# Optimization experiments

Measured on AMD Instinct MI355X. Metric: run time of the kernel, lower is better.

## Reference

```python
import jax, jax.numpy as jnp
from jax import lax
import numpy as np

NUM_BINS = 16
EPS = 1e-8


def setup_inputs() -> dict:
    key = jax.random.key(0)
    x = jax.random.normal(key, (32, 512, 4096), dtype=jnp.float32)
    return {"x": x}


def reference(x):
    B, C, L = x.shape  # [B, C, L]
    nb = NUM_BINS
    # g = mean over sequence -> [B, C]
    g = x.mean(axis=2)
    # cosine similarity along channel dim between each column x[:, :, l] and g
    dot = jnp.einsum('bcl,bc->bl', x, g)                      # [B, L]
    xn = jnp.sqrt(jnp.sum(x * x, axis=1))                     # [B, L]
    gn = jnp.sqrt(jnp.sum(g * g, axis=1, keepdims=True))      # [B, 1]
    cos = dot / jnp.maximum(xn * gn, EPS)                     # [B, L]
    S = cos.reshape(-1)                                       # [B*L]
    # torch.linspace on tensor endpoints detaches -> stop_gradient for fidelity
    min_S = lax.stop_gradient(S.min())
    max_S = lax.stop_gradient(S.max())
    levels = min_S + jnp.arange(nb, dtype=S.dtype) * (max_S - min_S) / (nb - 1)  # [nb]
    # soft triangular binning: (1 - |S - L_n|) inside a half-width 0.5/nb window
    d = jnp.abs(S[:, None] - levels[None, :])                 # [B*L, nb]
    E = jnp.where(d < 0.5 / nb, 1.0 - d, 0.0)
    E = E.reshape(B, L, nb)
    count_map = E.sum(axis=1)                                 # [B, nb]
    count_map = count_map / count_map.sum(axis=1, keepdims=True)
    # adaptive_avg_pool1d from length 1 to C//nb just replicates the value
    out = jnp.broadcast_to(count_map[:, :, None], (B, nb, C // nb))
    return out
```

## Files before the change

### kernel.cpp

```cpp
#include <hip/hip_runtime.h>

typedef float f4 __attribute__((ext_vector_type(4)));

#define BB 32
#define CC 512
#define LL 4096
#define NB 16
#define EPSF 1e-8f

__global__ __launch_bounds__(256, 2)
void k_main(const float* __restrict__ x, float* __restrict__ g,
            f4* __restrict__ pd4, f4* __restrict__ ps4) {
    __shared__ f4 ldsD[1024], ldsS[1024];
    const int tid = threadIdx.x;
    const int w = tid >> 6, lane = tid & 63;
    const int b  = blockIdx.x >> 4;
    const int c0 = (blockIdx.x & 15) * 32;

    f4 dA[16], sA[16];
#pragma unroll
    for (int i = 0; i < 16; ++i) { dA[i] = (f4)0.f; sA[i] = (f4)0.f; }

    const f4* base = (const f4*)(x + ((size_t)b * CC + c0 + w * 8) * LL);
    for (int cc = 0; cc < 8; ++cc) {
        const f4* row = base + (size_t)cc * 1024;
        f4 v[16];
#pragma unroll
        for (int i = 0; i < 16; ++i) v[i] = row[i * 64 + lane];
        float s = 0.f;
#pragma unroll
        for (int i = 0; i < 16; ++i) s += (v[i][0] + v[i][1]) + (v[i][2] + v[i][3]);
#pragma unroll
        for (int off = 32; off; off >>= 1) s += __shfl_down(s, off, 64);
        s = __shfl(s, 0, 64);
        const float gv = s * (1.0f / LL);
        if (lane == 0) g[b * CC + c0 + w * 8 + cc] = gv;
#pragma unroll
        for (int i = 0; i < 16; ++i) {
#pragma unroll
            for (int k = 0; k < 4; ++k) {
                dA[i][k] = fmaf(v[i][k], gv, dA[i][k]);
                sA[i][k] = fmaf(v[i][k], v[i][k], sA[i][k]);
            }
        }
    }
    for (int ww = 0; ww < 4; ++ww) {
        if (w == ww) {
#pragma unroll
            for (int i = 0; i < 16; ++i) {
                const int idx = i * 64 + lane;
                if (ww == 0) { ldsD[idx] = dA[i];  ldsS[idx] = sA[i]; }
                else         { ldsD[idx] += dA[i]; ldsS[idx] += sA[i]; }
            }
        }
        __syncthreads();
    }
#pragma unroll
    for (int j = 0; j < 4; ++j) {
        pd4[(size_t)blockIdx.x * 1024 + j * 256 + tid] = ldsD[j * 256 + tid];
        ps4[(size_t)blockIdx.x * 1024 + j * 256 + tid] = ldsS[j * 256 + tid];
    }
}

__global__ __launch_bounds__(256, 8)
void k_reduce(const float* __restrict__ g,
              const f4* __restrict__ pd4, const f4* __restrict__ ps4,
              f4* __restrict__ cosv4,
              float* __restrict__ pmin, float* __restrict__ pmax) {
    const int tid = threadIdx.x;
    const int w = tid >> 6, lane = tid & 63;
    const int b = blockIdx.x >> 4;
    const int sl = (blockIdx.x & 15) * 64 + lane;

    f4 pdv = (f4)0.f, psv = (f4)0.f;
    const size_t cb = (size_t)b * 16;
#pragma unroll
    for (int c = 0; c < 4; ++c) {
        const int ch = 4 * w + c;
        pdv += pd4[((cb + ch) << 10) + sl];
        psv += ps4[((cb + ch) << 10) + sl];
    }
    __shared__ f4 sD[4][64], sS[4][64];
    sD[w][lane] = pdv;
    sS[w][lane] = psv;

    const f4* g4p = (const f4*)(g + b * CC);
    f4 ga = g4p[lane], gb2 = g4p[64 + lane];
    float sq = 0.f;
#pragma unroll
    for (int k = 0; k < 4; ++k) sq = fmaf(ga[k], ga[k], fmaf(gb2[k], gb2[k], sq));
#pragma unroll
    for (int off = 32; off; off >>= 1) sq += __shfl_down(sq, off, 64);
    const float gn = sqrtf(__shfl(sq, 0, 64));

    __syncthreads();
    if (tid < 64) {
        f4 d = ((sD[0][lane] + sD[1][lane]) + sD[2][lane]) + sD[3][lane];
        f4 ssum = ((sS[0][lane] + sS[1][lane]) + sS[2][lane]) + sS[3][lane];
        f4 cs;
#pragma unroll
        for (int k = 0; k < 4; ++k)
            cs[k] = d[k] / fmaxf(sqrtf(ssum[k]) * gn, EPSF);
        cosv4[(size_t)b * 1024 + sl] = cs;

        float mn = fminf(fminf(cs[0], cs[1]), fminf(cs[2], cs[3]));
        float mx = fmaxf(fmaxf(cs[0], cs[1]), fmaxf(cs[2], cs[3]));
#pragma unroll
        for (int off = 32; off; off >>= 1) {
            mn = fminf(mn, __shfl_down(mn, off, 64));
            mx = fmaxf(mx, __shfl_down(mx, off, 64));
        }
        if (lane == 0) { pmin[blockIdx.x] = mn; pmax[blockIdx.x] = mx; }
    }
}

__global__ void k_hist(const float* __restrict__ cosv,
                       const float* __restrict__ pmin, const float* __restrict__ pmax,
                       float* __restrict__ out) {
    const int b = blockIdx.x;
    const int wave = threadIdx.x >> 6, lane = threadIdx.x & 63;

    float mn = fminf(pmin[threadIdx.x], pmin[threadIdx.x + 256]);
    float mx = fmaxf(pmax[threadIdx.x], pmax[threadIdx.x + 256]);
#pragma unroll
    for (int off = 32; off; off >>= 1) {
        mn = fminf(mn, __shfl_down(mn, off, 64));
        mx = fmaxf(mx, __shfl_down(mx, off, 64));
    }
    __shared__ float smn[4], smx[4];
    if (lane == 0) { smn[wave] = mn; smx[wave] = mx; }
    __syncthreads();
    mn = fminf(fminf(smn[0], smn[1]), fminf(smn[2], smn[3]));
    mx = fmaxf(fmaxf(smx[0], smx[1]), fmaxf(smx[2], smx[3]));
    const float range = mx - mn;

    float bins[NB];
#pragma unroll
    for (int n = 0; n < NB; ++n) bins[n] = 0.f;

    const float* cb = cosv + (b << 12);
    for (int l = threadIdx.x; l < LL; l += 256) {
        float s = cb[l];
#pragma unroll
        for (int n = 0; n < NB; ++n) {
            float lev = mn + ((float)n * range) / 15.0f;
            float d = fabsf(s - lev);
            bins[n] += (d < 0.03125f) ? (1.0f - d) : 0.f;
        }
    }
#pragma unroll
    for (int n = 0; n < NB; ++n) {
#pragma unroll
        for (int off = 32; off; off >>= 1) bins[n] += __shfl_down(bins[n], off, 64);
    }
    __shared__ float sb[4][NB];
    if (lane == 0) {
#pragma unroll
        for (int n = 0; n < NB; ++n) sb[wave][n] = bins[n];
    }
    __syncthreads();
    __shared__ float colsum[NB];
    if (threadIdx.x < NB) {
        const int n = threadIdx.x;
        colsum[n] = sb[0][n] + sb[1][n] + sb[2][n] + sb[3][n];
    }
    __syncthreads();
    float total = 0.f;
#pragma unroll
    for (int n = 0; n < NB; ++n) total += colsum[n];
    {
        const int i0 = threadIdx.x;
        out[b * (NB * 32) + i0]       = colsum[i0 >> 5] / total;
        out[b * (NB * 32) + i0 + 256] = colsum[(i0 + 256) >> 5] / total;
    }
}

extern "C" void kernel_launch(void* const* d_in, const int* in_sizes, int n_in,
                              void* d_out, int out_size, void* d_ws, size_t ws_size,
                              hipStream_t stream) {
    const float* x = (const float*)d_in[0];
    float* out = (float*)d_out;
    float* ws  = (float*)d_ws;

    float* g    = ws;
    float* cosv = ws + 16384;
    float* pmin = ws + 16384 + 131072;
    float* pmax = pmin + 512;
    f4*    pd4  = (f4*)(pmax + 512);
    f4*    ps4  = pd4 + 524288;

    k_main<<<512, 256, 0, stream>>>(x, g, pd4, ps4);
    k_reduce<<<512, 256, 0, stream>>>(g, pd4, ps4, (f4*)cosv, pmin, pmax);
    k_hist<<<32, 256, 0, stream>>>(cosv, pmin, pmax, out);
}
```

Baseline: 66.09 us.

## Prefetch next channel row via register double-buffering with LDS staging

```diff
diff --git a/kernel.cpp b/kernel.cpp
--- a/kernel.cpp
+++ b/kernel.cpp
@@ -11,7 +11,7 @@
 __global__ __launch_bounds__(256, 2)
 void k_main(const float* __restrict__ x, float* __restrict__ g,
             f4* __restrict__ pd4, f4* __restrict__ ps4) {
-    __shared__ f4 ldsD[1024], ldsS[1024];
+    __shared__ f4 buf[4][1024];
     const int tid = threadIdx.x;
     const int w = tid >> 6, lane = tid & 63;
     const int b  = blockIdx.x >> 4;
@@ -22,14 +22,28 @@
     for (int i = 0; i < 16; ++i) { dA[i] = (f4)0.f; sA[i] = (f4)0.f; }
 
     const f4* base = (const f4*)(x + ((size_t)b * CC + c0 + w * 8) * LL);
+    f4* wb = buf[w];
+
+    f4 v[16];
+#pragma unroll
+    for (int i = 0; i < 16; ++i) v[i] = base[i * 64 + lane];
+
     for (int cc = 0; cc < 8; ++cc) {
-        const f4* row = base + (size_t)cc * 1024;
-        f4 v[16];
-#pragma unroll
-        for (int i = 0; i < 16; ++i) v[i] = row[i * 64 + lane];
         float s = 0.f;
 #pragma unroll
-        for (int i = 0; i < 16; ++i) s += (v[i][0] + v[i][1]) + (v[i][2] + v[i][3]);
+        for (int i = 0; i < 16; ++i) {
+            wb[i * 64 + lane] = v[i];
+#pragma unroll
+            for (int k = 0; k < 4; ++k)
+                sA[i][k] = fmaf(v[i][k], v[i][k], sA[i][k]);
+            s += (v[i][0] + v[i][1]) + (v[i][2] + v[i][3]);
+        }
+        if (cc < 7) {
+            const f4* nr = base + (size_t)(cc + 1) * 1024;
+#pragma unroll
+            for (int i = 0; i < 16; ++i) v[i] = nr[i * 64 + lane];
+        }
+        __builtin_amdgcn_sched_barrier(0);
 #pragma unroll
         for (int off = 32; off; off >>= 1) s += __shfl_down(s, off, 64);
         s = __shfl(s, 0, 64);
@@ -37,13 +51,15 @@
         if (lane == 0) g[b * CC + c0 + w * 8 + cc] = gv;
 #pragma unroll
         for (int i = 0; i < 16; ++i) {
-#pragma unroll
-            for (int k = 0; k < 4; ++k) {
-                dA[i][k] = fmaf(v[i][k], gv, dA[i][k]);
-                sA[i][k] = fmaf(v[i][k], v[i][k], sA[i][k]);
-            }
-        }
-    }
+            f4 f = wb[i * 64 + lane];
+#pragma unroll
+            for (int k = 0; k < 4; ++k)
+                dA[i][k] = fmaf(f[k], gv, dA[i][k]);
+        }
+    }
+    __syncthreads();
+    f4* ldsD = &buf[0][0];
+    f4* ldsS = &buf[2][0];
     for (int ww = 0; ww < 4; ++ww) {
         if (w == ww) {
 #pragma unroll
@@ -114,7 +130,7 @@
     }
 }
 
-__global__ void k_hist(const float* __restrict__ cosv,
+__global__ void k_hist(const f4* __restrict__ cosv4,
                        const float* __restrict__ pmin, const float* __restrict__ pmax,
                        float* __restrict__ out) {
     const int b = blockIdx.x;
@@ -138,14 +154,19 @@
 #pragma unroll
     for (int n = 0; n < NB; ++n) bins[n] = 0.f;
 
-    const float* cb = cosv + (b << 12);
-    for (int l = threadIdx.x; l < LL; l += 256) {
-        float s = cb[l];
-#pragma unroll
-        for (int n = 0; n < NB; ++n) {
-            float lev = mn + ((float)n * range) / 15.0f;
-            float d = fabsf(s - lev);
-            bins[n] += (d < 0.03125f) ? (1.0f - d) : 0.f;
+    const f4* cb = cosv4 + b * 1024;
+#pragma unroll
+    for (int j = 0; j < 4; ++j) {
+        f4 sv = cb[j * 256 + threadIdx.x];
+#pragma unroll
+        for (int k = 0; k < 4; ++k) {
+            const float s = sv[k];
+#pragma unroll
+            for (int n = 0; n < NB; ++n) {
+                float lev = mn + ((float)n * range) / 15.0f;
+                float d = fabsf(s - lev);
+                bins[n] += (d < 0.03125f) ? (1.0f - d) : 0.f;
+            }
         }
     }
 #pragma unroll
@@ -191,5 +212,5 @@
 
     k_main<<<512, 256, 0, stream>>>(x, g, pd4, ps4);
     k_reduce<<<512, 256, 0, stream>>>(g, pd4, ps4, (f4*)cosv, pmin, pmax);
-    k_hist<<<32, 256, 0, stream>>>(cosv, pmin, pmax, out);
-}
+    k_hist<<<32, 256, 0, stream>>>((const f4*)cosv, pmin, pmax, out);
+}
```

After: 98.15 us. 48.5% more time.

## Fuse reduce and histogram kernels using a grid-wide atomic barrier

Applied to the files above, without the earlier changes.

```diff
diff --git a/kernel.cpp b/kernel.cpp
--- a/kernel.cpp
+++ b/kernel.cpp
@@ -62,27 +62,22 @@
     }
 }
 
-__global__ __launch_bounds__(256, 8)
-void k_reduce(const float* __restrict__ g,
-              const f4* __restrict__ pd4, const f4* __restrict__ ps4,
-              f4* __restrict__ cosv4,
-              float* __restrict__ pmin, float* __restrict__ pmax) {
+__global__ __launch_bounds__(1024, 1)
+void k_rh(const float* __restrict__ g,
+          const f4* __restrict__ pd4, const f4* __restrict__ ps4,
+          float* __restrict__ pmin, float* __restrict__ pmax,
+          unsigned* __restrict__ counter, float* __restrict__ out) {
+    const int b = blockIdx.x;
     const int tid = threadIdx.x;
     const int w = tid >> 6, lane = tid & 63;
-    const int b = blockIdx.x >> 4;
-    const int sl = (blockIdx.x & 15) * 64 + lane;
 
     f4 pdv = (f4)0.f, psv = (f4)0.f;
     const size_t cb = (size_t)b * 16;
 #pragma unroll
-    for (int c = 0; c < 4; ++c) {
-        const int ch = 4 * w + c;
-        pdv += pd4[((cb + ch) << 10) + sl];
-        psv += ps4[((cb + ch) << 10) + sl];
+    for (int ch = 0; ch < 16; ++ch) {
+        pdv += pd4[((cb + ch) << 10) + tid];
+        psv += ps4[((cb + ch) << 10) + tid];
     }
-    __shared__ f4 sD[4][64], sS[4][64];
-    sD[w][lane] = pdv;
-    sS[w][lane] = psv;
 
     const f4* g4p = (const f4*)(g + b * CC);
     f4 ga = g4p[lane], gb2 = g4p[64 + lane];
@@ -93,57 +88,55 @@
     for (int off = 32; off; off >>= 1) sq += __shfl_down(sq, off, 64);
     const float gn = sqrtf(__shfl(sq, 0, 64));
 
-    __syncthreads();
-    if (tid < 64) {
-        f4 d = ((sD[0][lane] + sD[1][lane]) + sD[2][lane]) + sD[3][lane];
-        f4 ssum = ((sS[0][lane] + sS[1][lane]) + sS[2][lane]) + sS[3][lane];
-        f4 cs;
+    f4 cs;
 #pragma unroll
-        for (int k = 0; k < 4; ++k)
-            cs[k] = d[k] / fmaxf(sqrtf(ssum[k]) * gn, EPSF);
-        cosv4[(size_t)b * 1024 + sl] = cs;
+    for (int k = 0; k < 4; ++k)
+        cs[k] = pdv[k] / fmaxf(sqrtf(psv[k]) * gn, EPSF);
 
-        float mn = fminf(fminf(cs[0], cs[1]), fminf(cs[2], cs[3]));
-        float mx = fmaxf(fmaxf(cs[0], cs[1]), fmaxf(cs[2], cs[3]));
-#pragma unroll
-        for (int off = 32; off; off >>= 1) {
-            mn = fminf(mn, __shfl_down(mn, off, 64));
-            mx = fmaxf(mx, __shfl_down(mx, off, 64));
-        }
-        if (lane == 0) { pmin[blockIdx.x] = mn; pmax[blockIdx.x] = mx; }
-    }
-}
-
-__global__ void k_hist(const float* __restrict__ cosv,
-                       const float* __restrict__ pmin, const float* __restrict__ pmax,
-                       float* __restrict__ out) {
-    const int b = blockIdx.x;
-    const int wave = threadIdx.x >> 6, lane = threadIdx.x & 63;
-
-    float mn = fminf(pmin[threadIdx.x], pmin[threadIdx.x + 256]);
-    float mx = fmaxf(pmax[threadIdx.x], pmax[threadIdx.x + 256]);
+    float mn = fminf(fminf(cs[0], cs[1]), fminf(cs[2], cs[3]));
+    float mx = fmaxf(fmaxf(cs[0], cs[1]), fmaxf(cs[2], cs[3]));
 #pragma unroll
     for (int off = 32; off; off >>= 1) {
         mn = fminf(mn, __shfl_down(mn, off, 64));
         mx = fmaxf(mx, __shfl_down(mx, off, 64));
     }
-    __shared__ float smn[4], smx[4];
-    if (lane == 0) { smn[wave] = mn; smx[wave] = mx; }
+    __shared__ float smn[16], smx[16];
+    if (lane == 0) { smn[w] = mn; smx[w] = mx; }
     __syncthreads();
-    mn = fminf(fminf(smn[0], smn[1]), fminf(smn[2], smn[3]));
-    mx = fmaxf(fmaxf(smx[0], smx[1]), fmaxf(smx[2], smx[3]));
-    const float range = mx - mn;
+    if (tid == 0) {
+        float bmn = smn[0], bmx = smx[0];
+#pragma unroll
+        for (int i = 1; i < 16; ++i) { bmn = fminf(bmn, smn[i]); bmx = fmaxf(bmx, smx[i]); }
+        pmin[b] = bmn; pmax[b] = bmx;
+        __threadfence();
+        atomicAdd(counter, 1u);
+    }
+    if (tid == 0) {
+        while (__hip_atomic_load(counter, __ATOMIC_ACQUIRE, __HIP_MEMORY_SCOPE_AGENT) < 32u)
+            __builtin_amdgcn_s_sleep(2);
+    }
+    __syncthreads();
+
+    __shared__ float lmn[32], lmx[32];
+    if (tid < 32) {
+        lmn[tid] = __hip_atomic_load(&pmin[tid], __ATOMIC_RELAXED, __HIP_MEMORY_SCOPE_AGENT);
+        lmx[tid] = __hip_atomic_load(&pmax[tid], __ATOMIC_RELAXED, __HIP_MEMORY_SCOPE_AGENT);
+    }
+    __syncthreads();
+    float gmn = lmn[0], gmx = lmx[0];
+#pragma unroll
+    for (int i = 1; i < 32; ++i) { gmn = fminf(gmn, lmn[i]); gmx = fmaxf(gmx, lmx[i]); }
+    const float range = gmx - gmn;
 
     float bins[NB];
 #pragma unroll
     for (int n = 0; n < NB; ++n) bins[n] = 0.f;
-
-    const float* cb = cosv + (b << 12);
-    for (int l = threadIdx.x; l < LL; l += 256) {
-        float s = cb[l];
+#pragma unroll
+    for (int k = 0; k < 4; ++k) {
+        const float s = cs[k];
 #pragma unroll
         for (int n = 0; n < NB; ++n) {
-            float lev = mn + ((float)n * range) / 15.0f;
+            float lev = gmn + ((float)n * range) / 15.0f;
             float d = fabsf(s - lev);
             bins[n] += (d < 0.03125f) ? (1.0f - d) : 0.f;
         }
@@ -153,25 +146,25 @@
 #pragma unroll
         for (int off = 32; off; off >>= 1) bins[n] += __shfl_down(bins[n], off, 64);
     }
-    __shared__ float sb[4][NB];
+    __shared__ float sb[16][NB];
     if (lane == 0) {
 #pragma unroll
-        for (int n = 0; n < NB; ++n) sb[wave][n] = bins[n];
+        for (int n = 0; n < NB; ++n) sb[w][n] = bins[n];
     }
     __syncthreads();
     __shared__ float colsum[NB];
-    if (threadIdx.x < NB) {
-        const int n = threadIdx.x;
-        colsum[n] = sb[0][n] + sb[1][n] + sb[2][n] + sb[3][n];
+    if (tid < NB) {
+        float c = 0.f;
+#pragma unroll
+        for (int i = 0; i < 16; ++i) c += sb[i][tid];
+        colsum[tid] = c;
     }
     __syncthreads();
-    float total = 0.f;
+    if (tid < NB * 32) {
+        float total = 0.f;
 #pragma unroll
-    for (int n = 0; n < NB; ++n) total += colsum[n];
-    {
-        const int i0 = threadIdx.x;
-        out[b * (NB * 32) + i0]       = colsum[i0 >> 5] / total;
-        out[b * (NB * 32) + i0 + 256] = colsum[(i0 + 256) >> 5] / total;
+        for (int n = 0; n < NB; ++n) total += colsum[n];
+        out[b * (NB * 32) + tid] = colsum[tid >> 5] / total;
     }
 }
 
@@ -182,14 +175,14 @@
     float* out = (float*)d_out;
     float* ws  = (float*)d_ws;
 
-    float* g    = ws;
-    float* cosv = ws + 16384;
-    float* pmin = ws + 16384 + 131072;
-    float* pmax = pmin + 512;
-    f4*    pd4  = (f4*)(pmax + 512);
-    f4*    ps4  = pd4 + 524288;
+    float*    g       = ws;
+    float*    pmin    = ws + 16384;
+    float*    pmax    = ws + 16384 + 64;
+    unsigned* counter = (unsigned*)(ws + 16384 + 128);
+    f4*       pd4     = (f4*)(ws + 16384 + 256);
+    f4*       ps4     = pd4 + 524288;
 
+    hipMemsetAsync(counter, 0, sizeof(unsigned), stream);
     k_main<<<512, 256, 0, stream>>>(x, g, pd4, ps4);
-    k_reduce<<<512, 256, 0, stream>>>(g, pd4, ps4, (f4*)cosv, pmin, pmax);
-    k_hist<<<32, 256, 0, stream>>>(cosv, pmin, pmax, out);
+    k_rh<<<32, 1024, 0, stream>>>(g, pd4, ps4, pmin, pmax, counter, out);
 }
```

Measured after the change: 74.17 us. 1.12x slower.

## Fuse reduce and histogram kernels using grid-wide atomic barriers

Applied to the files above, without the earlier changes.

```diff
diff --git a/kernel.cpp b/kernel.cpp
--- a/kernel.cpp
+++ b/kernel.cpp
@@ -62,11 +62,12 @@
     }
 }
 
-__global__ __launch_bounds__(256, 8)
-void k_reduce(const float* __restrict__ g,
-              const f4* __restrict__ pd4, const f4* __restrict__ ps4,
-              f4* __restrict__ cosv4,
-              float* __restrict__ pmin, float* __restrict__ pmax) {
+__global__ __launch_bounds__(256)
+void k_rh(const float* __restrict__ g,
+          const f4* __restrict__ pd4, const f4* __restrict__ ps4,
+          float* __restrict__ pmin, float* __restrict__ pmax,
+          float* __restrict__ bblk, unsigned* __restrict__ counters,
+          float* __restrict__ out) {
     const int tid = threadIdx.x;
     const int w = tid >> 6, lane = tid & 63;
     const int b = blockIdx.x >> 4;
@@ -94,82 +95,94 @@
     const float gn = sqrtf(__shfl(sq, 0, 64));
 
     __syncthreads();
+    f4 cs = (f4)0.f;
+    float mn = 1e30f, mx = -1e30f;
     if (tid < 64) {
         f4 d = ((sD[0][lane] + sD[1][lane]) + sD[2][lane]) + sD[3][lane];
         f4 ssum = ((sS[0][lane] + sS[1][lane]) + sS[2][lane]) + sS[3][lane];
-        f4 cs;
 #pragma unroll
         for (int k = 0; k < 4; ++k)
             cs[k] = d[k] / fmaxf(sqrtf(ssum[k]) * gn, EPSF);
-        cosv4[(size_t)b * 1024 + sl] = cs;
-
-        float mn = fminf(fminf(cs[0], cs[1]), fminf(cs[2], cs[3]));
-        float mx = fmaxf(fmaxf(cs[0], cs[1]), fmaxf(cs[2], cs[3]));
+        mn = fminf(fminf(cs[0], cs[1]), fminf(cs[2], cs[3]));
+        mx = fmaxf(fmaxf(cs[0], cs[1]), fmaxf(cs[2], cs[3]));
 #pragma unroll
         for (int off = 32; off; off >>= 1) {
             mn = fminf(mn, __shfl_down(mn, off, 64));
             mx = fmaxf(mx, __shfl_down(mx, off, 64));
         }
-        if (lane == 0) { pmin[blockIdx.x] = mn; pmax[blockIdx.x] = mx; }
-    }
-}
-
-__global__ void k_hist(const float* __restrict__ cosv,
-                       const float* __restrict__ pmin, const float* __restrict__ pmax,
-                       float* __restrict__ out) {
-    const int b = blockIdx.x;
-    const int wave = threadIdx.x >> 6, lane = threadIdx.x & 63;
-
-    float mn = fminf(pmin[threadIdx.x], pmin[threadIdx.x + 256]);
-    float mx = fmaxf(pmax[threadIdx.x], pmax[threadIdx.x + 256]);
+    }
+    if (tid == 0) {
+        pmin[blockIdx.x] = mn;
+        pmax[blockIdx.x] = mx;
+        __threadfence();
+        atomicAdd(&counters[0], 1u);
+        while (__hip_atomic_load(&counters[0], __ATOMIC_ACQUIRE, __HIP_MEMORY_SCOPE_AGENT) < 512u)
+            __builtin_amdgcn_s_sleep(2);
+    }
+    __syncthreads();
+
+    float m0 = fminf(pmin[tid], pmin[tid + 256]);
+    float m1 = fmaxf(pmax[tid], pmax[tid + 256]);
 #pragma unroll
     for (int off = 32; off; off >>= 1) {
-        mn = fminf(mn, __shfl_down(mn, off, 64));
-        mx = fmaxf(mx, __shfl_down(mx, off, 64));
+        m0 = fminf(m0, __shfl_down(m0, off, 64));
+        m1 = fmaxf(m1, __shfl_down(m1, off, 64));
     }
     __shared__ float smn[4], smx[4];
-    if (lane == 0) { smn[wave] = mn; smx[wave] = mx; }
-    __syncthreads();
-    mn = fminf(fminf(smn[0], smn[1]), fminf(smn[2], smn[3]));
-    mx = fmaxf(fmaxf(smx[0], smx[1]), fmaxf(smx[2], smx[3]));
-    const float range = mx - mn;
-
-    float bins[NB];
-#pragma unroll
-    for (int n = 0; n < NB; ++n) bins[n] = 0.f;
-
-    const float* cb = cosv + (b << 12);
-    for (int l = threadIdx.x; l < LL; l += 256) {
-        float s = cb[l];
+    if (lane == 0) { smn[w] = m0; smx[w] = m1; }
+    __syncthreads();
+    const float gmn = fminf(fminf(smn[0], smn[1]), fminf(smn[2], smn[3]));
+    const float gmx = fmaxf(fmaxf(smx[0], smx[1]), fmaxf(smx[2], smx[3]));
+    const float range = gmx - gmn;
+
+    if (tid < 64) {
+        float bins[NB];
+#pragma unroll
+        for (int n = 0; n < NB; ++n) bins[n] = 0.f;
+#pragma unroll
+        for (int k = 0; k < 4; ++k) {
+            const float s = cs[k];
+#pragma unroll
+            for (int n = 0; n < NB; ++n) {
+                float lev = gmn + ((float)n * range) / 15.0f;
+                float d = fabsf(s - lev);
+                bins[n] += (d < 0.03125f) ? (1.0f - d) : 0.f;
+            }
+        }
 #pragma unroll
         for (int n = 0; n < NB; ++n) {
-            float lev = mn + ((float)n * range) / 15.0f;
-            float d = fabsf(s - lev);
-            bins[n] += (d < 0.03125f) ? (1.0f - d) : 0.f;
-        }
-    }
-#pragma unroll
-    for (int n = 0; n < NB; ++n) {
-#pragma unroll
-        for (int off = 32; off; off >>= 1) bins[n] += __shfl_down(bins[n], off, 64);
-    }
-    __shared__ float sb[4][NB];
-    if (lane == 0) {
-#pragma unroll
-        for (int n = 0; n < NB; ++n) sb[wave][n] = bins[n];
-    }
-    __syncthreads();
+#pragma unroll
+            for (int off = 32; off; off >>= 1) bins[n] += __shfl_down(bins[n], off, 64);
+        }
+        if (lane == 0) {
+#pragma unroll
+            for (int n = 0; n < NB; ++n) bblk[blockIdx.x * NB + n] = bins[n];
+            __threadfence();
+            atomicAdd(&counters[1], 1u);
+        }
+    }
+    if ((blockIdx.x & 15) != 0) return;
+
+    if (tid == 0) {
+        while (__hip_atomic_load(&counters[1], __ATOMIC_ACQUIRE, __HIP_MEMORY_SCOPE_AGENT) < 512u)
+            __builtin_amdgcn_s_sleep(2);
+    }
+    __syncthreads();
+
     __shared__ float colsum[NB];
-    if (threadIdx.x < NB) {
-        const int n = threadIdx.x;
-        colsum[n] = sb[0][n] + sb[1][n] + sb[2][n] + sb[3][n];
+    if (tid < NB) {
+        float c = 0.f;
+#pragma unroll
+        for (int ch = 0; ch < 16; ++ch)
+            c += bblk[(b * 16 + ch) * NB + tid];
+        colsum[tid] = c;
     }
     __syncthreads();
     float total = 0.f;
 #pragma unroll
     for (int n = 0; n < NB; ++n) total += colsum[n];
     {
-        const int i0 = threadIdx.x;
+        const int i0 = tid;
         out[b * (NB * 32) + i0]       = colsum[i0 >> 5] / total;
         out[b * (NB * 32) + i0 + 256] = colsum[(i0 + 256) >> 5] / total;
     }
@@ -182,14 +195,16 @@
     float* out = (float*)d_out;
     float* ws  = (float*)d_ws;
 
-    float* g    = ws;
-    float* cosv = ws + 16384;
-    float* pmin = ws + 16384 + 131072;
-    float* pmax = pmin + 512;
-    f4*    pd4  = (f4*)(pmax + 512);
-    f4*    ps4  = pd4 + 524288;
-
+    float*    g        = ws;
+    float*    pmin     = ws + 16384;
+    float*    pmax     = pmin + 512;
+    unsigned* counters = (unsigned*)(pmax + 512);
+    float*    bblk     = (float*)(counters + 16);
+    f4*       pd4      = (f4*)(bblk + 8192);
+    f4*       ps4      = pd4 + 524288;
+
+    hipMemsetAsync(counters, 0, 64, stream);
     k_main<<<512, 256, 0, stream>>>(x, g, pd4, ps4);
-    k_reduce<<<512, 256, 0, stream>>>(g, pd4, ps4, (f4*)cosv, pmin, pmax);
-    k_hist<<<32, 256, 0, stream>>>(cosv, pmin, pmax, out);
+    k_rh<<<512, 256, 0, stream>>>(g, pd4, ps4, pmin, pmax, bblk,
+                                  counters, out);
 }
```

New measurement: 112.8 us. 70.7% more time.
